# Kernel optimization log

Measured on AMD Instinct MI355X. Metric: run time of the kernel, lower is better.

The kernel has to match this reference:

```python
import jax, jax.numpy as jnp
import numpy as np

N = 1_000_000          # total nodes (atoms)
F = 32                 # node feature dim
K = 16                 # kernels per degree
DEG_COUNTS = [200_000, 300_000, 300_000, 200_000]  # focal nodes per degree 1..4
EPS = 1e-8


def _unit(a):
    # L2-normalize along last axis (CosineSimilarity semantics)
    return a / (jnp.linalg.norm(a, axis=-1, keepdims=True) + EPS)


def setup_inputs() -> dict:
    key = jax.random.key(0)
    ks = jax.random.split(key, 16)
    x = jax.random.normal(ks[0], (N, F), dtype=jnp.float32)
    # selected indices: disjoint partition of all nodes by degree (a permutation)
    perm = jax.random.permutation(ks[1], N)
    sels, off = [], 0
    for c in DEG_COUNTS:
        sels.append(perm[off:off + c].astype(jnp.int64))
        off += c
    inp = {"x": x}
    for d in range(1, 5):
        inp[f"selected_index_deg{d}"] = sels[d - 1]
        inp[f"nei_index_deg{d}"] = jax.random.randint(
            ks[1 + d], (d * DEG_COUNTS[d - 1],), 0, N).astype(jnp.int64)
        inp[f"W_focal{d}"] = jax.random.normal(ks[7 + d], (K, F), dtype=jnp.float32)
        inp[f"W_nei{d}"] = jax.random.normal(ks[11 + d], (K, d, F), dtype=jnp.float32)
    return inp


def _degree_score(x, sel, nei, Wf, Wn, deg):
    # gather receptive field for this degree group
    x_focal = _unit(x[sel])                         # (Nd, F)
    x_nei = _unit(x[nei].reshape(-1, deg, F))       # (Nd, deg, F)
    sc_f = _unit(Wf) @ x_focal.T                    # (K, Nd) cosine vs focal kernel
    sc_n = jnp.einsum('kdf,ndf->kn', _unit(Wn), x_nei) / deg  # mean neighbor cosine
    return sc_f + sc_n                              # (K, Nd)


def reference(x,
              W_focal1, W_nei1, W_focal2, W_nei2,
              W_focal3, W_nei3, W_focal4, W_nei4,
              selected_index_deg1, selected_index_deg2,
              selected_index_deg3, selected_index_deg4,
              nei_index_deg1, nei_index_deg2,
              nei_index_deg3, nei_index_deg4):
    sels = [selected_index_deg1, selected_index_deg2,
            selected_index_deg3, selected_index_deg4]
    neis = [nei_index_deg1, nei_index_deg2, nei_index_deg3, nei_index_deg4]
    Wfs = [W_focal1, W_focal2, W_focal3, W_focal4]
    Wns = [W_nei1, W_nei2, W_nei3, W_nei4]

    out = jnp.zeros((4 * K, N), dtype=x.dtype)  # the `zeros` score matrix
    row, col = 0, 0
    for d in range(1, 5):
        sc = _degree_score(x, sels[d - 1], neis[d - 1], Wfs[d - 1], Wns[d - 1], d)
        nd = sels[d - 1].shape[0]
        out = out.at[row:row + K, col:col + nd].set(sc)
        row += K
        col += nd
    # reorder columns back to original node order (get_reorder_index -> sort)
    order = jnp.argsort(jnp.concatenate(sels))
    return out[:, order].T  # (N, 4*K)
```

## Files before the change

### kernel.cpp

```cpp
#include <hip/hip_runtime.h>
#include <math.h>

#define F 32
#define K 16
#define EPSN 1e-8f


typedef _Float16 half8 __attribute__((ext_vector_type(8)));
typedef float f32x4  __attribute__((ext_vector_type(4)));

template<int DEG>
__device__ __forceinline__ void process_deg(const float* __restrict__ x,
                                            const int*   __restrict__ sel,
                                            const int*   __restrict__ nei,
                                            const float* __restrict__ Wf,
                                            const float* __restrict__ Wn,
                                            float* __restrict__ out,
                                            int nd, int i0,
                                            _Float16* sWh, _Float16* sWl)
{
    constexpr int R  = 1 + DEG;
    constexpr int NW = K * R;
    const int tid = threadIdx.x;

    if (tid < NW) {
        const float* src = (tid < K) ? (Wf + tid * F) : (Wn + (tid - K) * F);
        float ss = 0.f;
        #pragma unroll
        for (int f = 0; f < F; ++f) { const float t = src[f]; ss += t * t; }
        const float sc = 1.f / (sqrtf(ss) + EPSN);
        const int t = tid - K;
        const int r = (tid < K) ? 0   : (1 + t % DEG);
        const int k = (tid < K) ? tid : (t / DEG);
        #pragma unroll
        for (int f = 0; f < F; ++f) {
            const float wv = src[f] * sc;
            const _Float16 hi = (_Float16)wv;
            const _Float16 lo = (_Float16)(wv - (float)hi);
            const int off = r * 512 + (k + 16 * (f >> 3)) * 8 + (f & 7);
            sWh[off] = hi; sWl[off] = lo;
        }
    }
    __syncthreads();

    const int lane = tid & 63;
    const int wv   = tid >> 6;
    const int jcol = lane & 15;
    const int kq   = lane >> 4;
    const float invdeg = 1.f / (float)DEG;

    #pragma unroll 1
    for (int it = 0; it < 4; ++it) {
        int i = i0 + it * 64 + wv * 16 + jcol;
        const bool valid = (i < nd);
        if (!valid) i = nd - 1;

        const int node = sel[i];
        int nn[DEG];
        #pragma unroll
        for (int j = 0; j < DEG; ++j) nn[j] = nei[i * DEG + j];

        f32x4 acc = {0.f, 0.f, 0.f, 0.f};

        #pragma unroll
        for (int r = 0; r < R; ++r) {
            const unsigned row = (unsigned)((r == 0) ? node : nn[r - 1]);
            const float* xr = x + row * (unsigned)F + kq * 8;
            const float4 a0 = *(const float4*)(xr);
            const float4 a1 = *(const float4*)(xr + 4);

            float ss = a0.x*a0.x + a0.y*a0.y + a0.z*a0.z + a0.w*a0.w
                     + a1.x*a1.x + a1.y*a1.y + a1.z*a1.z + a1.w*a1.w;
            ss += __shfl_xor(ss, 16);
            ss += __shfl_xor(ss, 32);
            float sc = 1.f / (sqrtf(ss) + EPSN);
            if (r > 0) sc *= invdeg;

            const float f0 = a0.x*sc, f1 = a0.y*sc, f2 = a0.z*sc, f3 = a0.w*sc;
            const float f4 = a1.x*sc, f5 = a1.y*sc, f6 = a1.z*sc, f7 = a1.w*sc;

            half8 bh, bl;
            bh[0]=(_Float16)f0; bl[0]=(_Float16)(f0-(float)bh[0]);
            bh[1]=(_Float16)f1; bl[1]=(_Float16)(f1-(float)bh[1]);
            bh[2]=(_Float16)f2; bl[2]=(_Float16)(f2-(float)bh[2]);
            bh[3]=(_Float16)f3; bl[3]=(_Float16)(f3-(float)bh[3]);
            bh[4]=(_Float16)f4; bl[4]=(_Float16)(f4-(float)bh[4]);
            bh[5]=(_Float16)f5; bl[5]=(_Float16)(f5-(float)bh[5]);
            bh[6]=(_Float16)f6; bl[6]=(_Float16)(f6-(float)bh[6]);
            bh[7]=(_Float16)f7; bl[7]=(_Float16)(f7-(float)bh[7]);

            const int aoff = r * 512 + lane * 8;
            const half8 ah = *(const half8*)(sWh + aoff);
            const half8 al = *(const half8*)(sWl + aoff);

            acc = __builtin_amdgcn_mfma_f32_16x16x32_f16(ah, bh, acc, 0, 0, 0);
            acc = __builtin_amdgcn_mfma_f32_16x16x32_f16(ah, bl, acc, 0, 0, 0);
            acc = __builtin_amdgcn_mfma_f32_16x16x32_f16(al, bh, acc, 0, 0, 0);
        }

        if (valid) {
            float* orow = out + (size_t)node * (4 * K);
            #pragma unroll
            for (int b = 0; b < 4; ++b) {
                float4 vst = make_float4(0.f, 0.f, 0.f, 0.f);
                if (b == DEG - 1)
                    vst = make_float4(acc[0], acc[1], acc[2], acc[3]);
                *(float4*)(orow + (b * 4 + kq) * 4) = vst;
            }
        }
    }
}

struct Args {
    const float* x;
    const int*   sel[4];
    const int*   nei[4];
    const float* Wf[4];
    const float* Wn[4];
    int nd[4];
    int bcum[4];
};

__global__ __launch_bounds__(256)
void fused_kernel(Args a, float* __restrict__ out)
{
    __shared__ __align__(16) _Float16 sWh[5 * 512];
    __shared__ __align__(16) _Float16 sWl[5 * 512];
    const int bid = blockIdx.x;

    if (bid < a.bcum[0]) {
        process_deg<1>(a.x, a.sel[0], a.nei[0], a.Wf[0], a.Wn[0], out,
                       a.nd[0], bid * 256, sWh, sWl);
    } else if (bid < a.bcum[1]) {
        process_deg<2>(a.x, a.sel[1], a.nei[1], a.Wf[1], a.Wn[1], out,
                       a.nd[1], (bid - a.bcum[0]) * 256, sWh, sWl);
    } else if (bid < a.bcum[2]) {
        process_deg<3>(a.x, a.sel[2], a.nei[2], a.Wf[2], a.Wn[2], out,
                       a.nd[2], (bid - a.bcum[1]) * 256, sWh, sWl);
    } else {
        process_deg<4>(a.x, a.sel[3], a.nei[3], a.Wf[3], a.Wn[3], out,
                       a.nd[3], (bid - a.bcum[2]) * 256, sWh, sWl);
    }
}

extern "C" void kernel_launch(void* const* d_in, const int* in_sizes, int n_in,
                              void* d_out, int out_size, void* d_ws, size_t ws_size,
                              hipStream_t stream)
{
    Args a;
    a.x = (const float*)d_in[0];
    for (int d = 0; d < 4; ++d) {
        a.sel[d] = (const int*)  d_in[1 + 4 * d];
        a.nei[d] = (const int*)  d_in[2 + 4 * d];
        a.Wf[d]  = (const float*)d_in[3 + 4 * d];
        a.Wn[d]  = (const float*)d_in[4 + 4 * d];
        a.nd[d]  = in_sizes[1 + 4 * d];
    }
    int cum = 0;
    for (int d = 0; d < 4; ++d) {
        cum += (a.nd[d] + 255) / 256;
        a.bcum[d] = cum;
    }
    float* out = (float*)d_out;
    fused_kernel<<<cum, 256, 0, stream>>>(a, out);
}
```

Before: 443.0 us.

## Prefetch next iteration's indices and batch row loads; double nodes per block

Software-pipelines the per-wave loop: all feature-row loads for an iteration are issued up front, and the sel/nei indices for the next iteration are fetched before the compute phase. A scheduling barrier keeps the compiler from reordering loads past the compute. Each block now covers 512 nodes instead of 256, which halves the grid and amortizes the per-block weight normalization into shared memory. The trade-off is higher register pressure and fewer blocks for latency hiding on a gather-bound kernel.

```diff
diff --git a/kernel.cpp b/kernel.cpp
--- a/kernel.cpp
+++ b/kernel.cpp
@@ -4,6 +4,7 @@
 #define F 32
 #define K 16
 #define EPSN 1e-8f
+#define NPB 512
 
 
 typedef _Float16 half8 __attribute__((ext_vector_type(8)));
@@ -19,8 +20,9 @@
                                             int nd, int i0,
                                             _Float16* sWh, _Float16* sWl)
 {
-    constexpr int R  = 1 + DEG;
-    constexpr int NW = K * R;
+    constexpr int R     = 1 + DEG;
+    constexpr int NW    = K * R;
+    constexpr int ITERS = NPB / 64;
     const int tid = threadIdx.x;
 
     if (tid < NW) {
@@ -49,25 +51,43 @@
     const int kq   = lane >> 4;
     const float invdeg = 1.f / (float)DEG;
 
+    int i = i0 + wv * 16 + jcol;
+    int ic = (i < nd) ? i : (nd - 1);
+    int node = sel[ic];
+    int nn[DEG];
+    #pragma unroll
+    for (int j = 0; j < DEG; ++j) nn[j] = nei[ic * DEG + j];
+
     #pragma unroll 1
-    for (int it = 0; it < 4; ++it) {
-        int i = i0 + it * 64 + wv * 16 + jcol;
-        const bool valid = (i < nd);
-        if (!valid) i = nd - 1;
-
-        const int node = sel[i];
-        int nn[DEG];
-        #pragma unroll
-        for (int j = 0; j < DEG; ++j) nn[j] = nei[i * DEG + j];
-
-        f32x4 acc = {0.f, 0.f, 0.f, 0.f};
-
+    for (int it = 0; it < ITERS; ++it) {
+        float4 rv[2 * R];
         #pragma unroll
         for (int r = 0; r < R; ++r) {
             const unsigned row = (unsigned)((r == 0) ? node : nn[r - 1]);
             const float* xr = x + row * (unsigned)F + kq * 8;
-            const float4 a0 = *(const float4*)(xr);
-            const float4 a1 = *(const float4*)(xr + 4);
+            rv[2 * r]     = *(const float4*)(xr);
+            rv[2 * r + 1] = *(const float4*)(xr + 4);
+        }
+
+        int node_n = node;
+        int nn_n[DEG];
+        #pragma unroll
+        for (int j = 0; j < DEG; ++j) nn_n[j] = nn[j];
+        if (it + 1 < ITERS) {
+            const int i2  = i0 + (it + 1) * 64 + wv * 16 + jcol;
+            const int ic2 = (i2 < nd) ? i2 : (nd - 1);
+            node_n = sel[ic2];
+            #pragma unroll
+            for (int j = 0; j < DEG; ++j) nn_n[j] = nei[ic2 * DEG + j];
+        }
+
+        __builtin_amdgcn_sched_barrier(0);
+
+        f32x4 acc = {0.f, 0.f, 0.f, 0.f};
+        #pragma unroll
+        for (int r = 0; r < R; ++r) {
+            const float4 a0 = rv[2 * r];
+            const float4 a1 = rv[2 * r + 1];
 
             float ss = a0.x*a0.x + a0.y*a0.y + a0.z*a0.z + a0.w*a0.w
                      + a1.x*a1.x + a1.y*a1.y + a1.z*a1.z + a1.w*a1.w;
@@ -98,7 +118,7 @@
             acc = __builtin_amdgcn_mfma_f32_16x16x32_f16(al, bh, acc, 0, 0, 0);
         }
 
-        if (valid) {
+        if (i0 + it * 64 + wv * 16 + jcol < nd) {
             float* orow = out + (size_t)node * (4 * K);
             #pragma unroll
             for (int b = 0; b < 4; ++b) {
@@ -108,6 +128,10 @@
                 *(float4*)(orow + (b * 4 + kq) * 4) = vst;
             }
         }
+
+        node = node_n;
+        #pragma unroll
+        for (int j = 0; j < DEG; ++j) nn[j] = nn_n[j];
     }
 }
 
@@ -130,16 +154,16 @@
 
     if (bid < a.bcum[0]) {
         process_deg<1>(a.x, a.sel[0], a.nei[0], a.Wf[0], a.Wn[0], out,
-                       a.nd[0], bid * 256, sWh, sWl);
+                       a.nd[0], bid * NPB, sWh, sWl);
     } else if (bid < a.bcum[1]) {
         process_deg<2>(a.x, a.sel[1], a.nei[1], a.Wf[1], a.Wn[1], out,
-                       a.nd[1], (bid - a.bcum[0]) * 256, sWh, sWl);
+                       a.nd[1], (bid - a.bcum[0]) * NPB, sWh, sWl);
     } else if (bid < a.bcum[2]) {
         process_deg<3>(a.x, a.sel[2], a.nei[2], a.Wf[2], a.Wn[2], out,
-                       a.nd[2], (bid - a.bcum[1]) * 256, sWh, sWl);
+                       a.nd[2], (bid - a.bcum[1]) * NPB, sWh, sWl);
     } else {
         process_deg<4>(a.x, a.sel[3], a.nei[3], a.Wf[3], a.Wn[3], out,
-                       a.nd[3], (bid - a.bcum[2]) * 256, sWh, sWl);
+                       a.nd[3], (bid - a.bcum[2]) * NPB, sWh, sWl);
     }
 }
 
@@ -158,7 +182,7 @@
     }
     int cum = 0;
     for (int d = 0; d < 4; ++d) {
-        cum += (a.nd[d] + 255) / 256;
+        cum += (a.nd[d] + NPB - 1) / NPB;
         a.bcum[d] = cum;
     }
     float* out = (float*)d_out;
```

Measured after the change: 443.5 us. Within noise of the previous version (+0.1%).

## Software-pipeline index and row gathers with inline asm loads and explicit vmcnt waits

Applied to the files above, without the earlier changes.

Restructures the per-wave loop into a software pipeline. Index loads for the next two iterations and the feature-row gathers for the next node are issued before the current node's normalization and MFMA work, with explicit s_waitcnt vmcnt counts bounding the overlap. Each block now covers 512 nodes instead of 256, which amortizes the per-block weight normalization, and launch bounds request 2 blocks per SIMD. The risks are higher register pressure, fragile hand-counted vmcnt values, and fewer blocks for load balancing.

```diff
diff --git a/kernel.cpp b/kernel.cpp
--- a/kernel.cpp
+++ b/kernel.cpp
@@ -4,10 +4,94 @@
 #define F 32
 #define K 16
 #define EPSN 1e-8f
+#define NPB 512
 
 
 typedef _Float16 half8 __attribute__((ext_vector_type(8)));
 typedef float f32x4  __attribute__((ext_vector_type(4)));
+typedef int   i32x2  __attribute__((ext_vector_type(2)));
+typedef int   i32x4  __attribute__((ext_vector_type(4)));
+
+#define VMWAIT(N) do { asm volatile("s_waitcnt vmcnt(%0)" :: "n"(N) : "memory"); \
+                       __builtin_amdgcn_sched_barrier(0); } while (0)
+
+__device__ __forceinline__ void gpair(f32x4& a, f32x4& b, const float* x,
+                                      unsigned row, int kq) {
+    const unsigned off = row * 128u + (unsigned)kq * 32u;
+    asm volatile("global_load_dwordx4 %0, %1, %2"
+                 : "=&v"(a) : "v"(off), "s"(x) : "memory");
+    asm volatile("global_load_dwordx4 %0, %1, %2 offset:16"
+                 : "=&v"(b) : "v"(off), "s"(x) : "memory");
+}
+
+__device__ __forceinline__ void gstore(float* out, unsigned off, f32x4 v) {
+    asm volatile("global_store_dwordx4 %0, %1, %2"
+                 :: "v"(off), "v"(v), "s"(out) : "memory");
+}
+
+template<int DEG> struct Idx;
+template<> struct Idx<1> { int node; int n0;
+    __device__ __forceinline__ int nb(int) const { return n0; } };
+template<> struct Idx<2> { int node; i32x2 nn;
+    __device__ __forceinline__ int nb(int j) const { return nn[j]; } };
+template<> struct Idx<3> { int node; i32x2 nn; int n2;
+    __device__ __forceinline__ int nb(int j) const { return j < 2 ? nn[j] : n2; } };
+template<> struct Idx<4> { int node; i32x4 nn;
+    __device__ __forceinline__ int nb(int j) const { return nn[j]; } };
+
+template<int DEG>
+__device__ __forceinline__ void load_idx(Idx<DEG>& d, const int* sel,
+                                         const int* nei, int ic) {
+    const unsigned so = (unsigned)ic << 2;
+    asm volatile("global_load_dword %0, %1, %2"
+                 : "=&v"(d.node) : "v"(so), "s"(sel) : "memory");
+    const unsigned no = (unsigned)(ic * DEG) << 2;
+    if constexpr (DEG == 1)
+        asm volatile("global_load_dword %0, %1, %2"
+                     : "=&v"(d.n0) : "v"(no), "s"(nei) : "memory");
+    else if constexpr (DEG == 2)
+        asm volatile("global_load_dwordx2 %0, %1, %2"
+                     : "=&v"(d.nn) : "v"(no), "s"(nei) : "memory");
+    else if constexpr (DEG == 3) {
+        asm volatile("global_load_dwordx2 %0, %1, %2"
+                     : "=&v"(d.nn) : "v"(no), "s"(nei) : "memory");
+        asm volatile("global_load_dword %0, %1, %2 offset:8"
+                     : "=&v"(d.n2) : "v"(no), "s"(nei) : "memory");
+    } else
+        asm volatile("global_load_dwordx4 %0, %1, %2"
+                     : "=&v"(d.nn) : "v"(no), "s"(nei) : "memory");
+}
+
+template<int DEG>
+__device__ __forceinline__ f32x4 slab_compute(f32x4 a, f32x4 b, f32x4 acc,
+                                              const _Float16* sWh,
+                                              const _Float16* sWl,
+                                              int lane, int r) {
+    float ss = a[0]*a[0] + a[1]*a[1] + a[2]*a[2] + a[3]*a[3]
+             + b[0]*b[0] + b[1]*b[1] + b[2]*b[2] + b[3]*b[3];
+    ss += __shfl_xor(ss, 16);
+    ss += __shfl_xor(ss, 32);
+    float sc = 1.f / (sqrtf(ss) + EPSN);
+    if (r > 0) sc *= (1.f / (float)DEG);
+    const float f0 = a[0]*sc, f1 = a[1]*sc, f2 = a[2]*sc, f3 = a[3]*sc;
+    const float f4 = b[0]*sc, f5 = b[1]*sc, f6 = b[2]*sc, f7 = b[3]*sc;
+    half8 bh, bl;
+    bh[0]=(_Float16)f0; bl[0]=(_Float16)(f0-(float)bh[0]);
+    bh[1]=(_Float16)f1; bl[1]=(_Float16)(f1-(float)bh[1]);
+    bh[2]=(_Float16)f2; bl[2]=(_Float16)(f2-(float)bh[2]);
+    bh[3]=(_Float16)f3; bl[3]=(_Float16)(f3-(float)bh[3]);
+    bh[4]=(_Float16)f4; bl[4]=(_Float16)(f4-(float)bh[4]);
+    bh[5]=(_Float16)f5; bl[5]=(_Float16)(f5-(float)bh[5]);
+    bh[6]=(_Float16)f6; bl[6]=(_Float16)(f6-(float)bh[6]);
+    bh[7]=(_Float16)f7; bl[7]=(_Float16)(f7-(float)bh[7]);
+    const int aoff = r * 512 + lane * 8;
+    const half8 ah = *(const half8*)(sWh + aoff);
+    const half8 al = *(const half8*)(sWl + aoff);
+    acc = __builtin_amdgcn_mfma_f32_16x16x32_f16(ah, bh, acc, 0, 0, 0);
+    acc = __builtin_amdgcn_mfma_f32_16x16x32_f16(ah, bl, acc, 0, 0, 0);
+    acc = __builtin_amdgcn_mfma_f32_16x16x32_f16(al, bh, acc, 0, 0, 0);
+    return acc;
+}
 
 template<int DEG>
 __device__ __forceinline__ void process_deg(const float* __restrict__ x,
@@ -19,8 +103,15 @@
                                             int nd, int i0,
                                             _Float16* sWh, _Float16* sWl)
 {
-    constexpr int R  = 1 + DEG;
+    constexpr int R  = DEG + 1;
+    constexpr int H  = (DEG <= 2) ? 1 : 2;
+    constexpr int C0 = 2 * H;
+    constexpr int C1 = 2 * (R - H);
+    constexpr int NI = (DEG == 3) ? 3 : 2;
+    constexpr int KB = C1 + NI;
+    constexpr int KD = C0;
     constexpr int NW = K * R;
+    constexpr int ITERS = NPB / 64;
     const int tid = threadIdx.x;
 
     if (tid < NW) {
@@ -47,68 +138,60 @@
     const int wv   = tid >> 6;
     const int jcol = lane & 15;
     const int kq   = lane >> 4;
-    const float invdeg = 1.f / (float)DEG;
+    const int i0w  = i0 + wv * 16 + jcol;
+
+    f32x4 g0[2 * H], g1[2 * (R - H)];
+    const f32x4 zed = {0.f, 0.f, 0.f, 0.f};
+
+    Idx<DEG> ix, iy;
+    { const int ic = (i0w < nd) ? i0w : (nd - 1);
+      load_idx<DEG>(ix, sel, nei, ic); }
+    { const int i1 = i0w + 64; const int ic = (i1 < nd) ? i1 : (nd - 1);
+      load_idx<DEG>(iy, sel, nei, ic); }
+    VMWAIT(NI);
+    #pragma unroll
+    for (int r = 0; r < H; ++r)
+        gpair(g0[2*r], g0[2*r+1], x,
+              (unsigned)((r == 0) ? ix.node : ix.nb(r-1)), kq);
+
+#define ITER(T, XC, YN)                                                        \
+    {                                                                          \
+        const int nodeT = XC.node;                                             \
+        _Pragma("unroll")                                                      \
+        for (int r = H; r < R; ++r)                        \
+            gpair(g1[2*(r-H)], g1[2*(r-H)+1], x, (unsigned)XC.nb(r-1), kq);    \
+        { const int ii = i0w + ((T) + 2) * 64;         \
+          load_idx<DEG>(XC, sel, nei, (ii < nd) ? ii : (nd - 1)); }            \
+        VMWAIT(KB);                            \
+        f32x4 acc = {0.f, 0.f, 0.f, 0.f};                                      \
+        _Pragma("unroll")                                                      \
+        for (int r = 0; r < H; ++r)                                            \
+            acc = slab_compute<DEG>(g0[2*r], g0[2*r+1], acc, sWh, sWl, lane, r);\
+        _Pragma("unroll")                                                      \
+        for (int r = 0; r < H; ++r)                      \
+            gpair(g0[2*r], g0[2*r+1], x,                                       \
+                  (unsigned)((r == 0) ? YN.node : YN.nb(r-1)), kq);            \
+        VMWAIT(KD);                                      \
+        _Pragma("unroll")                                                      \
+        for (int r = H; r < R; ++r)                                            \
+            acc = slab_compute<DEG>(g1[2*(r-H)], g1[2*(r-H)+1], acc,           \
+                                    sWh, sWl, lane, r);                        \
+        if (i0w + (T) * 64 < nd) {                           \
+            const unsigned ob = (unsigned)nodeT * 256u + (unsigned)kq * 16u;   \
+            _Pragma("unroll")                                                  \
+            for (int b = 0; b < 4; ++b)                                        \
+                gstore(out, ob + (unsigned)b * 64u,                            \
+                       (b == DEG - 1) ? acc : zed);                            \
+        }                                                                      \
+    }
 
     #pragma unroll 1
-    for (int it = 0; it < 4; ++it) {
-        int i = i0 + it * 64 + wv * 16 + jcol;
-        const bool valid = (i < nd);
-        if (!valid) i = nd - 1;
-
-        const int node = sel[i];
-        int nn[DEG];
-        #pragma unroll
-        for (int j = 0; j < DEG; ++j) nn[j] = nei[i * DEG + j];
-
-        f32x4 acc = {0.f, 0.f, 0.f, 0.f};
-
-        #pragma unroll
-        for (int r = 0; r < R; ++r) {
-            const unsigned row = (unsigned)((r == 0) ? node : nn[r - 1]);
-            const float* xr = x + row * (unsigned)F + kq * 8;
-            const float4 a0 = *(const float4*)(xr);
-            const float4 a1 = *(const float4*)(xr + 4);
-
-            float ss = a0.x*a0.x + a0.y*a0.y + a0.z*a0.z + a0.w*a0.w
-                     + a1.x*a1.x + a1.y*a1.y + a1.z*a1.z + a1.w*a1.w;
-            ss += __shfl_xor(ss, 16);
-            ss += __shfl_xor(ss, 32);
-            float sc = 1.f / (sqrtf(ss) + EPSN);
-            if (r > 0) sc *= invdeg;
-
-            const float f0 = a0.x*sc, f1 = a0.y*sc, f2 = a0.z*sc, f3 = a0.w*sc;
-            const float f4 = a1.x*sc, f5 = a1.y*sc, f6 = a1.z*sc, f7 = a1.w*sc;
-
-            half8 bh, bl;
-            bh[0]=(_Float16)f0; bl[0]=(_Float16)(f0-(float)bh[0]);
-            bh[1]=(_Float16)f1; bl[1]=(_Float16)(f1-(float)bh[1]);
-            bh[2]=(_Float16)f2; bl[2]=(_Float16)(f2-(float)bh[2]);
-            bh[3]=(_Float16)f3; bl[3]=(_Float16)(f3-(float)bh[3]);
-            bh[4]=(_Float16)f4; bl[4]=(_Float16)(f4-(float)bh[4]);
-            bh[5]=(_Float16)f5; bl[5]=(_Float16)(f5-(float)bh[5]);
-            bh[6]=(_Float16)f6; bl[6]=(_Float16)(f6-(float)bh[6]);
-            bh[7]=(_Float16)f7; bl[7]=(_Float16)(f7-(float)bh[7]);
-
-            const int aoff = r * 512 + lane * 8;
-            const half8 ah = *(const half8*)(sWh + aoff);
-            const half8 al = *(const half8*)(sWl + aoff);
-
-            acc = __builtin_amdgcn_mfma_f32_16x16x32_f16(ah, bh, acc, 0, 0, 0);
-            acc = __builtin_amdgcn_mfma_f32_16x16x32_f16(ah, bl, acc, 0, 0, 0);
-            acc = __builtin_amdgcn_mfma_f32_16x16x32_f16(al, bh, acc, 0, 0, 0);
-        }
-
-        if (valid) {
-            float* orow = out + (size_t)node * (4 * K);
-            #pragma unroll
-            for (int b = 0; b < 4; ++b) {
-                float4 vst = make_float4(0.f, 0.f, 0.f, 0.f);
-                if (b == DEG - 1)
-                    vst = make_float4(acc[0], acc[1], acc[2], acc[3]);
-                *(float4*)(orow + (b * 4 + kq) * 4) = vst;
-            }
-        }
-    }
+    for (int tp = 0; tp < ITERS; tp += 2) {
+        ITER(tp,     ix, iy);
+        ITER(tp + 1, iy, ix);
+    }
+#undef ITER
+    VMWAIT(0);
 }
 
 struct Args {
@@ -121,7 +204,7 @@
     int bcum[4];
 };
 
-__global__ __launch_bounds__(256)
+__global__ __launch_bounds__(256, 2)
 void fused_kernel(Args a, float* __restrict__ out)
 {
     __shared__ __align__(16) _Float16 sWh[5 * 512];
@@ -130,16 +213,16 @@
 
     if (bid < a.bcum[0]) {
         process_deg<1>(a.x, a.sel[0], a.nei[0], a.Wf[0], a.Wn[0], out,
-                       a.nd[0], bid * 256, sWh, sWl);
+                       a.nd[0], bid * NPB, sWh, sWl);
     } else if (bid < a.bcum[1]) {
         process_deg<2>(a.x, a.sel[1], a.nei[1], a.Wf[1], a.Wn[1], out,
-                       a.nd[1], (bid - a.bcum[0]) * 256, sWh, sWl);
+                       a.nd[1], (bid - a.bcum[0]) * NPB, sWh, sWl);
     } else if (bid < a.bcum[2]) {
         process_deg<3>(a.x, a.sel[2], a.nei[2], a.Wf[2], a.Wn[2], out,
-                       a.nd[2], (bid - a.bcum[1]) * 256, sWh, sWl);
+                       a.nd[2], (bid - a.bcum[1]) * NPB, sWh, sWl);
     } else {
         process_deg<4>(a.x, a.sel[3], a.nei[3], a.Wf[3], a.Wn[3], out,
-                       a.nd[3], (bid - a.bcum[2]) * 256, sWh, sWl);
+                       a.nd[3], (bid - a.bcum[2]) * NPB, sWh, sWl);
     }
 }
 
@@ -158,7 +241,7 @@
     }
     int cum = 0;
     for (int d = 0; d < 4; ++d) {
-        cum += (a.nd[d] + 255) / 256;
+        cum += (a.nd[d] + NPB - 1) / NPB;
         a.bcum[d] = cum;
     }
     float* out = (float*)d_out;
```

Result: no change. 447.7 us (+1.1%).
